# Optimization experiments

Hardware: AMD Instinct MI355X
Metric: run time of the kernel (lower is better)

Reference implementation:

```python
import jax, jax.numpy as jnp
import numpy as np

NUM_HEADS = 16


def setup_inputs() -> dict:
    key = jax.random.key(0)
    k1, k2, k3, k4 = jax.random.split(key, 4)
    in_dim, out_dim = 1024, 1024
    x = jax.random.normal(k1, (4, 2048, in_dim), dtype=jnp.float32)
    # nn.Linear weights stored as [out, in]; we keep that convention.
    s = 1.0 / np.sqrt(in_dim)
    Wq = jax.random.uniform(k2, (out_dim, in_dim), jnp.float32, -s, s)
    Wk = jax.random.uniform(k3, (out_dim, in_dim), jnp.float32, -s, s)
    Wv = jax.random.uniform(k4, (out_dim, in_dim), jnp.float32, -s, s)
    return {"x": x, "Wq": Wq, "Wk": Wk, "Wv": Wv}


def reference(x, Wq, Wk, Wv):
    b, n, _ = x.shape
    out_dim = Wq.shape[0]
    h = NUM_HEADS
    d = out_dim // h  # head_dim

    def split_heads(t):  # [b,n,out] -> [b,h,n,d]
        return t.reshape(b, n, h, d).transpose(0, 2, 1, 3)

    q = split_heads(x @ Wq.T)
    k = split_heads(x @ Wk.T)
    v = split_heads(x @ Wv.T)

    scores = jnp.einsum("bhqd,bhkd->bhqk", q, k) / jnp.sqrt(jnp.float32(d))
    causal = jnp.tril(jnp.ones((n, n), dtype=bool))
    scores = jnp.where(causal, scores, -jnp.inf)
    attn = jax.nn.softmax(scores, axis=-1)
    out = jnp.einsum("bhqk,bhkd->bhqd", attn, v)
    return out.transpose(0, 2, 1, 3).reshape(b, n, out_dim)
```

## Files before the change

kernel.cpp:

```cpp
#include <hip/hip_runtime.h>

typedef __attribute__((ext_vector_type(8))) short short8;
typedef __attribute__((ext_vector_type(4))) short short4v;
typedef __attribute__((ext_vector_type(4))) float floatx4;
typedef __attribute__((ext_vector_type(16))) float floatx16;
typedef __attribute__((ext_vector_type(2))) int iv2;

#define GLOBAL_AS __attribute__((address_space(1)))
#define LDS_AS __attribute__((address_space(3)))

__device__ __forceinline__ short f2bs(float f) {
    union { float f; unsigned u; } v; v.f = f;
    unsigned r = v.u + 0x7fffu + ((v.u >> 16) & 1u);
    return (short)(r >> 16);
}

#if __has_builtin(__builtin_amdgcn_cvt_pk_bf16_f32)
typedef __attribute__((ext_vector_type(2))) __bf16 bf16x2;
__device__ __forceinline__ unsigned pk2(float a, float b) {
    union { bf16x2 v; unsigned u; } u;
    u.v = __builtin_amdgcn_cvt_pk_bf16_f32(a, b);
    return u.u;
}
#else
__device__ __forceinline__ unsigned pk2(float a, float b) {
    union { float f; unsigned u; } x, y; x.f = a; y.f = b;
    return ((y.u + 0x8000u) & 0xffff0000u) | ((x.u + 0x8000u) >> 16);
}
#endif

__global__ __launch_bounds__(256) void cast_all(const float* __restrict__ x,
                                                const float* __restrict__ Wq,
                                                const float* __restrict__ Wk,
                                                const float* __restrict__ Wv,
                                                short* __restrict__ xb,
                                                short* __restrict__ wb) {
    int b = blockIdx.x;
    int t = threadIdx.x;
    const float* src;
    short* dst;
    int idx;
    if (b < 8192) {
        src = x; dst = xb; idx = b * 1024 + t * 4;
    } else {
        int r = b - 8192;
        int wz = r >> 10;
        src = (wz == 0) ? Wq : (wz == 1) ? Wk : Wv;
        dst = wb + wz * (1 << 20);
        idx = (r & 1023) * 1024 + t * 4;
    }
    float4 v = *(const float4*)(src + idx);
    short4v o;
    o.x = f2bs(v.x); o.y = f2bs(v.y); o.z = f2bs(v.z); o.w = f2bs(v.w);
    *(short4v*)(dst + idx) = o;
}

__global__ __launch_bounds__(256) void qkv_gemm(const short* __restrict__ xb,
                                                const short* __restrict__ wb,
                                                short* __restrict__ qout,
                                                short* __restrict__ kout,
                                                short* __restrict__ vtout) {
    __shared__ short As[128 * 64];
    __shared__ short Bs[128 * 64];
    const int K = 1024;
    int tid = threadIdx.x;
    int lane = tid & 63;
    int wid = tid >> 6;
    int quad = lane >> 4;
    int l16 = lane & 15;
    int wm = (wid >> 1) * 64;
    int wn = (wid & 1) * 64;
    int bm = blockIdx.x * 128;
    int bn = blockIdx.y * 128;
    const short* W = wb + (size_t)blockIdx.z * K * 1024;

    floatx4 acc[4][4];
#pragma unroll
    for (int i = 0; i < 4; i++)
#pragma unroll
        for (int j = 0; j < 4; j++) acc[i][j] = (floatx4){0.f, 0.f, 0.f, 0.f};

    int srow = tid >> 3;
    int ssw = ((tid & 7) ^ (srow & 7)) * 8;

    for (int kk = 0; kk < K; kk += 64) {
        __syncthreads();
#pragma unroll
        for (int l = 0; l < 4; l++) {
            const short* g = xb + (size_t)(bm + srow + l * 32) * K + kk + ssw;
            __builtin_amdgcn_global_load_lds((const GLOBAL_AS void*)g,
                                             (LDS_AS void*)(As + tid * 8 + l * 2048), 16, 0, 0);
        }
#pragma unroll
        for (int l = 0; l < 4; l++) {
            const short* g = W + (size_t)(bn + srow + l * 32) * K + kk + ssw;
            __builtin_amdgcn_global_load_lds((const GLOBAL_AS void*)g,
                                             (LDS_AS void*)(Bs + tid * 8 + l * 2048), 16, 0, 0);
        }
        __syncthreads();

#pragma unroll
        for (int s = 0; s < 2; s++) {
            int slot = ((s * 4 + quad) ^ (l16 & 7)) * 8;
            short8 af[4], bf[4];
#pragma unroll
            for (int i = 0; i < 4; i++)
                af[i] = *(const short8*)(As + (wm + i * 16 + l16) * 64 + slot);
#pragma unroll
            for (int j = 0; j < 4; j++)
                bf[j] = *(const short8*)(Bs + (wn + j * 16 + l16) * 64 + slot);
#pragma unroll
            for (int i = 0; i < 4; i++)
#pragma unroll
                for (int j = 0; j < 4; j++)
                    acc[i][j] = __builtin_amdgcn_mfma_f32_16x16x32_bf16(af[i], bf[j], acc[i][j], 0, 0, 0);
        }
    }

    if (blockIdx.z == 2) {
#pragma unroll
        for (int i = 0; i < 4; i++) {
#pragma unroll
            for (int j = 0; j < 4; j++) {
                int m = bm + wm + i * 16 + quad * 4;
                int c = bn + wn + j * 16 + l16;
                int b = m >> 11, nn = m & 2047, h = c >> 6, dd = c & 63;
                short4v pk;
                pk.x = f2bs(acc[i][j][0]);
                pk.y = f2bs(acc[i][j][1]);
                pk.z = f2bs(acc[i][j][2]);
                pk.w = f2bs(acc[i][j][3]);
                *(short4v*)(vtout + ((size_t)(b * 16 + h) * 64 + dd) * 2048 + nn) = pk;
            }
        }
    } else {
        short* dst = (blockIdx.z == 0) ? qout : kout;
        float qs = (blockIdx.z == 0) ? 0.180336881f : 1.0f;
#pragma unroll
        for (int i = 0; i < 4; i++) {
#pragma unroll
            for (int j = 0; j < 4; j++) {
#pragma unroll
                for (int r = 0; r < 4; r++) {
                    int m = bm + wm + i * 16 + quad * 4 + r;
                    int c = bn + wn + j * 16 + l16;
                    dst[((size_t)((m >> 11) * 16 + (c >> 6)) * 2048 + (m & 2047)) * 64 + (c & 63)] =
                        f2bs(acc[i][j][r] * qs);
                }
            }
        }
    }
}

__global__ __launch_bounds__(256, 2) void attn(const short* __restrict__ q,
                                               const short* __restrict__ k,
                                               const short* __restrict__ vt,
                                               float* __restrict__ out) {
    __shared__ short Ks[2][128 * 64];
    __shared__ short Vs[2][64 * 128];

    int tid = threadIdx.x;
    int lane = tid & 63;
    int wid = tid >> 6;
    int l32 = lane & 31;
    int half = lane >> 5;

    int flat = blockIdx.x;
    int xcd = flat & 7;
    int slot = flat >> 3;
    int bh = xcd * 8 + (slot >> 3);
    int qx = slot & 7;
    int b = bh >> 4, h = bh & 15;

    const short* qp = q + (size_t)(b * 16 + h) * 2048 * 64;
    const short* kp = k + (size_t)(b * 16 + h) * 2048 * 64;
    const short* vp = vt + (size_t)(b * 16 + h) * 64 * 2048;

    int krow = tid >> 3;
    int ksw = ((tid & 7) ^ (krow & 7)) * 8;
    int vd = tid >> 4;
    int vc = tid & 15;
    int vsw = ((vc & 8) | ((vc ^ vd) & 7)) * 8;

#define STAGE_KV(cb, kvb) do { \
    _Pragma("unroll") for (int l = 0; l < 4; l++) { \
        const short* g = kp + (size_t)((kvb) + krow + l * 32) * 64 + ksw; \
        __builtin_amdgcn_global_load_lds((const GLOBAL_AS void*)g, \
            (LDS_AS void*)(&Ks[cb][0] + tid * 8 + l * 2048), 16, 0, 0); \
    } \
    _Pragma("unroll") for (int l = 0; l < 4; l++) { \
        const short* g = vp + (size_t)(vd + l * 16) * 2048 + (kvb) + vsw; \
        __builtin_amdgcn_global_load_lds((const GLOBAL_AS void*)g, \
            (LDS_AS void*)(&Vs[cb][0] + tid * 8 + l * 2048), 16, 0, 0); \
    } \
} while (0)

    for (int phase = 0; phase < 2; phase++) {
        int qt = (phase == 0) ? qx : (15 - qx);
        int qbase = qt * 128;
        int qrow_w = qbase + wid * 32;
        int qlane = qrow_w + l32;

        short8 qf[4];
#pragma unroll
        for (int s = 0; s < 4; s++)
            qf[s] = *(const short8*)(qp + (size_t)qlane * 64 + s * 16 + half * 8);

        floatx16 oacc[2];
#pragma unroll
        for (int nt = 0; nt < 2; nt++)
#pragma unroll
            for (int e = 0; e < 16; e++) oacc[nt][e] = 0.f;
        float rs = 0.f;

        int ntiles = qt + 1;

        __builtin_amdgcn_sched_barrier(0);
        __builtin_amdgcn_s_barrier();
        __builtin_amdgcn_sched_barrier(0);
        STAGE_KV(0, 0);

        for (int t = 0; t < ntiles; t++) {
            int cur = t & 1;
            int kvb = t * 128;

            __builtin_amdgcn_sched_barrier(0);
            __builtin_amdgcn_s_barrier();
            __builtin_amdgcn_sched_barrier(0);
            if (t + 1 < ntiles) {
                STAGE_KV(cur ^ 1, kvb + 128);
                asm volatile("s_waitcnt vmcnt(8)" ::: "memory");
            } else {
                asm volatile("s_waitcnt vmcnt(0)" ::: "memory");
            }
            __builtin_amdgcn_sched_barrier(0);
            __builtin_amdgcn_s_barrier();
            __builtin_amdgcn_sched_barrier(0);

            const short* Kc = &Ks[cur][0];
            const short* Vc = &Vs[cur][0];

            floatx16 sacc[4];
#pragma unroll
            for (int kb = 0; kb < 4; kb++)
#pragma unroll
                for (int e = 0; e < 16; e++) sacc[kb][e] = 0.f;
#pragma unroll
            for (int s = 0; s < 4; s++) {
#pragma unroll
                for (int kb = 0; kb < 4; kb++) {
                    int key = kb * 32 + l32;
                    int c = s * 2 + half;
                    short8 kf = *(const short8*)(Kc + key * 64 + ((c ^ (key & 7)) * 8));
                    sacc[kb] = __builtin_amdgcn_mfma_f32_32x32x16_bf16(kf, qf[s], sacc[kb], 0, 0, 0);
                }
            }

            bool diag = (t == ntiles - 1) && (kvb + 127 > qrow_w);
            unsigned W0[4][4], W1[4][4];
#pragma unroll
            for (int kb = 0; kb < 4; kb++) {
#pragma unroll
                for (int e = 0; e < 16; e++) {
                    float p = __builtin_amdgcn_exp2f(sacc[kb][e]);
                    if (diag) {
                        int key = kvb + kb * 32 + (e & 3) + 8 * (e >> 2) + 4 * half;
                        p = (key > qlane) ? 0.f : p;
                    }
                    sacc[kb][e] = p;
                    rs += p;
                }
#pragma unroll
                for (int g = 0; g < 4; g++) {
                    W0[kb][g] = pk2(sacc[kb][4 * g + 0], sacc[kb][4 * g + 1]);
                    W1[kb][g] = pk2(sacc[kb][4 * g + 2], sacc[kb][4 * g + 3]);
                }
            }

#pragma unroll
            for (int s = 0; s < 8; s++) {
                int kb = s >> 1;
                int g0 = (s & 1) * 2;
                int g1 = g0 + 1;
                iv2 r0 = __builtin_amdgcn_permlane32_swap(W0[kb][g0], W0[kb][g1], false, false);
                iv2 r1 = __builtin_amdgcn_permlane32_swap(W1[kb][g0], W1[kb][g1], false, false);
                union { int4 v; short8 s8; } pu;
                pu.v.x = r0.x; pu.v.y = r1.x; pu.v.z = r0.y; pu.v.w = r1.y;
                short8 pf = pu.s8;
#pragma unroll
                for (int nt = 0; nt < 2; nt++) {
                    int d = nt * 32 + l32;
                    int c = s * 2 + half;
                    int sl = (c & 8) | ((c ^ (d & 7)) & 7);
                    short8 vf = *(const short8*)(Vc + d * 128 + sl * 8);
                    oacc[nt] = __builtin_amdgcn_mfma_f32_32x32x16_bf16(pf, vf, oacc[nt], 0, 0, 0);
                }
            }
        }

        float tot = rs + __shfl_xor(rs, 32);
        float inv = 1.0f / tot;
        float invr[16];
#pragma unroll
        for (int e = 0; e < 16; e++)
            invr[e] = __shfl(inv, (e & 3) + 8 * (e >> 2) + 4 * half);
#pragma unroll
        for (int nt = 0; nt < 2; nt++) {
#pragma unroll
            for (int e = 0; e < 16; e++) {
                int r = (e & 3) + 8 * (e >> 2) + 4 * half;
                int nn = qrow_w + r;
                out[((size_t)b * 2048 + nn) * 1024 + h * 64 + nt * 32 + l32] = oacc[nt][e] * invr[e];
            }
        }
    }
#undef STAGE_KV
}

extern "C" void kernel_launch(void* const* d_in, const int* in_sizes, int n_in,
                              void* d_out, int out_size, void* d_ws, size_t ws_size,
                              hipStream_t stream) {
    const float* x = (const float*)d_in[0];
    const float* Wq = (const float*)d_in[1];
    const float* Wk = (const float*)d_in[2];
    const float* Wv = (const float*)d_in[3];
    float* out = (float*)d_out;
    char* ws = (char*)d_ws;

    short* xb = (short*)ws;
    short* wb = (short*)(ws + (16u << 20));
    short* qb = (short*)(ws + (22u << 20));
    short* kb = (short*)(ws + (38u << 20));
    short* vtb = (short*)(ws + (54u << 20));

    cast_all<<<8192 + 3 * 1024, 256, 0, stream>>>(x, Wq, Wk, Wv, xb, wb);
    qkv_gemm<<<dim3(64, 8, 3), 256, 0, stream>>>(xb, wb, qb, kb, vtb);
    attn<<<512, 256, 0, stream>>>(qb, kb, vtb, out);
}
```

Baseline: 204.9 us.

## Double-buffer LDS tiles in QKV GEMM to overlap global loads with MFMA

```diff
diff --git a/kernel.cpp b/kernel.cpp
--- a/kernel.cpp
+++ b/kernel.cpp
@@ -60,8 +60,8 @@
                                                 short* __restrict__ qout,
                                                 short* __restrict__ kout,
                                                 short* __restrict__ vtout) {
-    __shared__ short As[128 * 64];
-    __shared__ short Bs[128 * 64];
+    __shared__ short As[2][128 * 64];
+    __shared__ short Bs[2][128 * 64];
     const int K = 1024;
     int tid = threadIdx.x;
     int lane = tid & 63;
@@ -83,32 +83,48 @@
     int srow = tid >> 3;
     int ssw = ((tid & 7) ^ (srow & 7)) * 8;
 
-    for (int kk = 0; kk < K; kk += 64) {
-        __syncthreads();
-#pragma unroll
-        for (int l = 0; l < 4; l++) {
-            const short* g = xb + (size_t)(bm + srow + l * 32) * K + kk + ssw;
-            __builtin_amdgcn_global_load_lds((const GLOBAL_AS void*)g,
-                                             (LDS_AS void*)(As + tid * 8 + l * 2048), 16, 0, 0);
-        }
-#pragma unroll
-        for (int l = 0; l < 4; l++) {
-            const short* g = W + (size_t)(bn + srow + l * 32) * K + kk + ssw;
-            __builtin_amdgcn_global_load_lds((const GLOBAL_AS void*)g,
-                                             (LDS_AS void*)(Bs + tid * 8 + l * 2048), 16, 0, 0);
-        }
-        __syncthreads();
-
+#define STAGE_AB(cb, kk) do { \
+    _Pragma("unroll") for (int l = 0; l < 4; l++) { \
+        const short* g = xb + (size_t)(bm + srow + l * 32) * K + (kk) + ssw; \
+        __builtin_amdgcn_global_load_lds((const GLOBAL_AS void*)g, \
+            (LDS_AS void*)(&As[cb][0] + tid * 8 + l * 2048), 16, 0, 0); \
+    } \
+    _Pragma("unroll") for (int l = 0; l < 4; l++) { \
+        const short* g = W + (size_t)(bn + srow + l * 32) * K + (kk) + ssw; \
+        __builtin_amdgcn_global_load_lds((const GLOBAL_AS void*)g, \
+            (LDS_AS void*)(&Bs[cb][0] + tid * 8 + l * 2048), 16, 0, 0); \
+    } \
+} while (0)
+
+    STAGE_AB(0, 0);
+
+    for (int T = 0; T < 16; T++) {
+        int cur = T & 1;
+        __builtin_amdgcn_sched_barrier(0);
+        __builtin_amdgcn_s_barrier();
+        __builtin_amdgcn_sched_barrier(0);
+        if (T < 15) {
+            STAGE_AB(cur ^ 1, (T + 1) * 64);
+            asm volatile("s_waitcnt vmcnt(8)" ::: "memory");
+        } else {
+            asm volatile("s_waitcnt vmcnt(0)" ::: "memory");
+        }
+        __builtin_amdgcn_sched_barrier(0);
+        __builtin_amdgcn_s_barrier();
+        __builtin_amdgcn_sched_barrier(0);
+
+        const short* Ac = &As[cur][0];
+        const short* Bc = &Bs[cur][0];
 #pragma unroll
         for (int s = 0; s < 2; s++) {
             int slot = ((s * 4 + quad) ^ (l16 & 7)) * 8;
             short8 af[4], bf[4];
 #pragma unroll
             for (int i = 0; i < 4; i++)
-                af[i] = *(const short8*)(As + (wm + i * 16 + l16) * 64 + slot);
+                af[i] = *(const short8*)(Ac + (wm + i * 16 + l16) * 64 + slot);
 #pragma unroll
             for (int j = 0; j < 4; j++)
-                bf[j] = *(const short8*)(Bs + (wn + j * 16 + l16) * 64 + slot);
+                bf[j] = *(const short8*)(Bc + (wn + j * 16 + l16) * 64 + slot);
 #pragma unroll
             for (int i = 0; i < 4; i++)
 #pragma unroll
@@ -116,6 +132,7 @@
                     acc[i][j] = __builtin_amdgcn_mfma_f32_16x16x32_bf16(af[i], bf[j], acc[i][j], 0, 0, 0);
         }
     }
+#undef STAGE_AB
 
     if (blockIdx.z == 2) {
 #pragma unroll
```

After: 199.8 us. 2.5% less time.
